# Optimization experiments

Hardware: AMD Instinct MI355X
Metric: run time of the kernel (lower is better)

## Reference

```python
import jax, jax.numpy as jnp
import numpy as np

N, NFEAT, NHID, NCLASS, NHEADS = 3072, 128, 64, 64, 8
ALPHA = 0.2  # LeakyReLU negative slope
NEG = -9e15  # masking value from pyGAT


def gat_layer(h, mask, W, a):
    # h: [N, Fin]; mask: [N, N] bool; W: [H, Fin, Fout]; a: [H, 2*Fout]
    fout = W.shape[-1]
    Wh = jnp.einsum('ni,hio->hno', h, W)            # [H, N, Fout]
    e_src = jnp.einsum('hno,ho->hn', Wh, a[:, :fout])
    e_dst = jnp.einsum('hno,ho->hn', Wh, a[:, fout:])
    e = jax.nn.leaky_relu(e_src[:, :, None] + e_dst[:, None, :], ALPHA)  # [H,N,N]
    e = jnp.where(mask[None], e, NEG)
    att = jax.nn.softmax(e, axis=-1)                 # dropout is identity in eval
    out = jnp.einsum('hnm,hmo->hno', att, Wh)        # [H, N, Fout]
    out = jax.nn.elu(out)                            # concat=True -> elu
    # concat heads along feature dim: [N, H*Fout]
    return out.transpose(1, 0, 2).reshape(h.shape[0], -1)


def setup_inputs() -> dict:
    key = jax.random.key(0)
    ks = jax.random.split(key, 10)
    x = jax.random.normal(ks[0], (N, NFEAT), dtype=jnp.float32)
    adj = (jax.random.uniform(ks[1], (N, N)) < 0.01).astype(jnp.float32)
    adj = jnp.maximum(adj, jnp.eye(N, dtype=jnp.float32))
    hid = NHID * NHEADS
    dims = [(NFEAT, NHID), (hid, NHID), (hid, NHID), (hid, NCLASS)]
    params = {}
    for i, (fin, fout) in enumerate(dims):
        kw, ka = jax.random.split(ks[2 + i])
        params[f'W{i+1}'] = jax.random.normal(kw, (NHEADS, fin, fout), dtype=jnp.float32) * (1.0 / np.sqrt(fin))
        params[f'a{i+1}'] = jax.random.normal(ka, (NHEADS, 2 * fout), dtype=jnp.float32) * 0.1
    return {'x': x, 'adj': adj, **params}


def reference(x, adj, W1, a1, W2, a2, W3, a3, W4, a4):
    mask = adj > 0
    h = gat_layer(x, mask, W1, a1)
    h = gat_layer(h, mask, W2, a2)
    h = gat_layer(h, mask, W3, a3)
    h = gat_layer(h, mask, W4, a4)
    return h  # [N, NHEADS*NCLASS]
```

## Files before the change

kernel.cpp:

```cpp
#include <hip/hip_runtime.h>
#include <math.h>

#define NN 3072
#define NH 8
#define FO 64
#define FCAT 512
#define MAXDEG 128
#define ALPHA 0.2f

typedef __attribute__((ext_vector_type(8))) short bf16x8;
typedef __attribute__((ext_vector_type(4))) float f32x4;

static __device__ __forceinline__ unsigned short f2bf(float v) {
    union { float f; unsigned u; } x; x.f = v;
    unsigned r = x.u + 0x7fffu + ((x.u >> 16) & 1u);
    return (unsigned short)(r >> 16);
}
static __device__ __forceinline__ float bf2f(unsigned short b) {
    union { unsigned u; float f; } x; x.u = ((unsigned)b) << 16;
    return x.f;
}

__global__ __launch_bounds__(256) void prelude_k(const float* __restrict__ x,
                                                 const float* __restrict__ adj,
                                                 const float* __restrict__ W1,
                                                 const float* __restrict__ W2,
                                                 const float* __restrict__ W3,
                                                 const float* __restrict__ W4,
                                                 unsigned short* __restrict__ Ah,
                                                 unsigned short* __restrict__ Al,
                                                 unsigned short* __restrict__ Wth,
                                                 unsigned short* __restrict__ Wtl,
                                                 int* __restrict__ deg,
                                                 int* __restrict__ nbr) {
    __shared__ float t[64][65];
    const int b = blockIdx.x, tid = threadIdx.x;

    if (b < 256) {
        int base = b * 1536 + tid;
        #pragma unroll
        for (int i = 0; i < 6; ++i) {
            int idx = base + i * 256;
            float v = x[idx];
            unsigned short hb = f2bf(v);
            Ah[idx] = hb;
            Al[idx] = f2bf(v - bf2f(hb));
        }
        if (b < 208) {
            const float* W; int K; int local; size_t obase;
            if (b < 16)       { W = W1; K = 128; local = b;       obase = 0; }
            else if (b < 80)  { W = W2; K = 512; local = b - 16;  obase = 65536; }
            else if (b < 144) { W = W3; K = 512; local = b - 80;  obase = 327680; }
            else              { W = W4; K = 512; local = b - 144; obase = 589824; }
            int nkt = K >> 6;
            int h = local / nkt, kt = local - h * nkt;
            int k0 = kt * 64;
            for (int idx = tid; idx < 4096; idx += 256) {
                int r = idx >> 6, c = idx & 63;
                t[r][c] = W[(size_t)h * K * FO + (size_t)(k0 + r) * FO + c];
            }
            __syncthreads();
            for (int idx = tid; idx < 4096; idx += 256) {
                int o = idx >> 6, kk = idx & 63;
                float v = t[kk][o];
                unsigned short hb = f2bf(v);
                size_t dst = obase + (size_t)(h * FO + o) * K + k0 + kk;
                Wth[dst] = hb;
                Wtl[dst] = f2bf(v - bf2f(hb));
            }
        }
    } else {
        int row = (b - 256) * 4 + (tid >> 6);
        int lane = tid & 63;
        const float* arow = adj + (size_t)row * NN;
        int count = 0;
        for (int base = 0; base < NN; base += 64) {
            float v = arow[base + lane];
            unsigned long long m = __ballot(v > 0.0f);
            if (v > 0.0f) {
                int pos = count + __popcll(m & ((1ull << lane) - 1ull));
                if (pos < MAXDEG) nbr[(size_t)row * MAXDEG + pos] = base + lane;
            }
            count += __popcll(m);
        }
        if (lane == 0) deg[row] = count < MAXDEG ? count : MAXDEG;
    }
}

__global__ __launch_bounds__(256, 3) void gemm_ee_k(const unsigned short* __restrict__ Ah,
                                                    const unsigned short* __restrict__ Al,
                                                    const unsigned short* __restrict__ Bh,
                                                    const unsigned short* __restrict__ Bl,
                                                    const float* __restrict__ a,
                                                    float* __restrict__ C,
                                                    float* __restrict__ esrc,
                                                    float* __restrict__ edst, int K) {
    __shared__ __align__(16) unsigned char smem[30720];
    typedef float CsT[68];
    unsigned short* As_ = (unsigned short*)smem;
    unsigned short* Bs_ = (unsigned short*)(smem + 10240);
    CsT* Cs = reinterpret_cast<CsT*>(smem);

    const int tid = threadIdx.x;
    const int h = blockIdx.x;
    const int r0 = blockIdx.y * 32;
    const int lane = tid & 63;
    const int wid = tid >> 6;
    const int wr = wid >> 1, wc = wid & 1;
    const int lr = lane & 15, lg = lane >> 4;

    const unsigned short* Bhh = Bh + (size_t)h * FO * K;
    const unsigned short* Bll = Bl + (size_t)h * FO * K;

    const int row0 = tid >> 3, cq0 = tid & 7;
    const int off0 = row0 * 80 + ((cq0 ^ (row0 & 7)) * 8);
    const size_t gA0 = (size_t)(r0 + row0) * K + cq0 * 8;
    const size_t gB0 = (size_t)row0 * K + cq0 * 8;
    const size_t gB1 = gB0 + (size_t)32 * K;

    bf16x8 rah, ral, rb0h, rb0l, rb1h, rb1l;

    auto loadg = [&](int k0) {
        rah = *(const bf16x8*)(Ah + gA0 + k0);
        ral = *(const bf16x8*)(Al + gA0 + k0);
        rb0h = *(const bf16x8*)(Bhh + gB0 + k0);
        rb0l = *(const bf16x8*)(Bll + gB0 + k0);
        rb1h = *(const bf16x8*)(Bhh + gB1 + k0);
        rb1l = *(const bf16x8*)(Bll + gB1 + k0);
    };
    auto store_lds = [&]() {
        *(bf16x8*)&As_[off0] = rah;
        *(bf16x8*)&As_[2560 + off0] = ral;
        *(bf16x8*)&Bs_[off0] = rb0h;
        *(bf16x8*)&Bs_[5120 + off0] = rb0l;
        *(bf16x8*)&Bs_[off0 + 2560] = rb1h;
        *(bf16x8*)&Bs_[5120 + off0 + 2560] = rb1l;
    };

    f32x4 acc[2];
    acc[0] = (f32x4){0.f, 0.f, 0.f, 0.f};
    acc[1] = (f32x4){0.f, 0.f, 0.f, 0.f};

    auto mfma_phase = [&]() {
        #pragma unroll
        for (int ks = 0; ks < 2; ++ks) {
            int cq = ks * 4 + lg;
            int arow = wr * 16 + lr;
            int offa = arow * 80 + ((cq ^ (arow & 7)) * 8);
            bf16x8 ah = *(const bf16x8*)&As_[offa];
            bf16x8 al = *(const bf16x8*)&As_[2560 + offa];
            bf16x8 bh[2], bl[2];
            #pragma unroll
            for (int j = 0; j < 2; ++j) {
                int col = wc * 32 + j * 16 + lr;
                int offb = col * 80 + ((cq ^ (col & 7)) * 8);
                bh[j] = *(const bf16x8*)&Bs_[offb];
                bl[j] = *(const bf16x8*)&Bs_[5120 + offb];
            }
            #pragma unroll
            for (int j = 0; j < 2; ++j) {
                acc[j] = __builtin_amdgcn_mfma_f32_16x16x32_bf16(ah, bh[j], acc[j], 0, 0, 0);
                acc[j] = __builtin_amdgcn_mfma_f32_16x16x32_bf16(ah, bl[j], acc[j], 0, 0, 0);
                acc[j] = __builtin_amdgcn_mfma_f32_16x16x32_bf16(al, bh[j], acc[j], 0, 0, 0);
            }
        }
    };

    loadg(0);
    store_lds();
    __syncthreads();
    for (int k0 = 64; k0 < K; k0 += 64) {
        loadg(k0);
        mfma_phase();
        __syncthreads();
        store_lds();
        __syncthreads();
    }
    mfma_phase();
    __syncthreads();

    #pragma unroll
    for (int j = 0; j < 2; ++j)
        #pragma unroll
        for (int r = 0; r < 4; ++r)
            Cs[wr * 16 + lg * 4 + r][wc * 32 + j * 16 + lr] = acc[j][r];
    __syncthreads();

    #pragma unroll
    for (int it = 0; it < 2; ++it) {
        int idx = tid + it * 256;
        int r = idx >> 4, c4 = idx & 15;
        *(float4*)&C[(size_t)(r0 + r) * FCAT + h * FO + c4 * 4] = *(float4*)&Cs[r][c4 * 4];
    }

    {
        int r = tid >> 3, sub = tid & 7;
        const float* av = a + h * 2 * FO;
        float s = 0.0f, dd = 0.0f;
        #pragma unroll
        for (int k = 0; k < 8; ++k) {
            float v = Cs[r][sub * 8 + k];
            s = fmaf(v, av[sub * 8 + k], s);
            dd = fmaf(v, av[FO + sub * 8 + k], dd);
        }
        s += __shfl_xor(s, 1); s += __shfl_xor(s, 2); s += __shfl_xor(s, 4);
        dd += __shfl_xor(dd, 1); dd += __shfl_xor(dd, 2); dd += __shfl_xor(dd, 4);
        if (sub == 0) {
            esrc[h * NN + r0 + r] = s;
            edst[h * NN + r0 + r] = dd;
        }
    }
}

__global__ __launch_bounds__(256) void attn_agg_k(const float* __restrict__ Wh,
                                                  const float* __restrict__ esrc,
                                                  const float* __restrict__ edst,
                                                  const int* __restrict__ deg,
                                                  const int* __restrict__ nbr,
                                                  float* __restrict__ outp,
                                                  unsigned short* __restrict__ oh,
                                                  unsigned short* __restrict__ ol,
                                                  int write_f32) {
    __shared__ float pbuf[4][MAXDEG];
    __shared__ int jbuf[4][MAXDEG];
    const int ws = threadIdx.x >> 6;
    const int lane = threadIdx.x & 63;
    const int h = blockIdx.x / (NN / 4);
    const int n = (blockIdx.x % (NN / 4)) * 4 + ws;
    const int d = deg[n];
    const int dpad = (d + 7) & ~7;
    const int* nb = nbr + (size_t)n * MAXDEG;
    const float es = esrc[h * NN + n];
    const float* ed = edst + h * NN;

    float lsum = 0.0f;
    for (int t = lane; t < dpad; t += 64) {
        int j = 0;
        float pv = 0.0f;
        if (t < d) {
            j = nb[t];
            float e = es + ed[j];
            e = (e > 0.0f) ? e : ALPHA * e;
            pv = __expf(e);
        }
        jbuf[ws][t] = j;
        pbuf[ws][t] = pv;
        lsum += pv;
    }
    #pragma unroll
    for (int off = 32; off; off >>= 1) lsum += __shfl_xor(lsum, off);

    const float* whb = Wh + h * FO + lane;
    float a0 = 0.f, a1 = 0.f, a2 = 0.f, a3 = 0.f;
    float a4 = 0.f, a5 = 0.f, a6 = 0.f, a7 = 0.f;
    for (int t = 0; t < dpad; t += 8) {
        a0 = fmaf(pbuf[ws][t + 0], whb[(size_t)jbuf[ws][t + 0] * FCAT], a0);
        a1 = fmaf(pbuf[ws][t + 1], whb[(size_t)jbuf[ws][t + 1] * FCAT], a1);
        a2 = fmaf(pbuf[ws][t + 2], whb[(size_t)jbuf[ws][t + 2] * FCAT], a2);
        a3 = fmaf(pbuf[ws][t + 3], whb[(size_t)jbuf[ws][t + 3] * FCAT], a3);
        a4 = fmaf(pbuf[ws][t + 4], whb[(size_t)jbuf[ws][t + 4] * FCAT], a4);
        a5 = fmaf(pbuf[ws][t + 5], whb[(size_t)jbuf[ws][t + 5] * FCAT], a5);
        a6 = fmaf(pbuf[ws][t + 6], whb[(size_t)jbuf[ws][t + 6] * FCAT], a6);
        a7 = fmaf(pbuf[ws][t + 7], whb[(size_t)jbuf[ws][t + 7] * FCAT], a7);
    }
    float acc = ((a0 + a1) + (a2 + a3)) + ((a4 + a5) + (a6 + a7));
    acc /= lsum;
    float r = (acc > 0.0f) ? acc : (__expf(acc) - 1.0f);
    size_t idx = (size_t)n * FCAT + h * FO + lane;
    if (write_f32) {
        outp[idx] = r;
    } else {
        unsigned short hb = f2bf(r);
        oh[idx] = hb;
        ol[idx] = f2bf(r - bf2f(hb));
    }
}

extern "C" void kernel_launch(void* const* d_in, const int* in_sizes, int n_in,
                              void* d_out, int out_size, void* d_ws, size_t ws_size,
                              hipStream_t stream) {
    const float* x   = (const float*)d_in[0];
    const float* adj = (const float*)d_in[1];
    const float* ap[4] = {(const float*)d_in[3], (const float*)d_in[5],
                          (const float*)d_in[7], (const float*)d_in[9]};
    float* out = (float*)d_out;

    char* p = (char*)d_ws;
    int* deg = (int*)p;              p += (size_t)NN * sizeof(int);
    int* nbr = (int*)p;              p += (size_t)NN * MAXDEG * sizeof(int);
    unsigned short* Ah = (unsigned short*)p; p += (size_t)NN * FCAT * 2;
    unsigned short* Al = (unsigned short*)p; p += (size_t)NN * FCAT * 2;
    float* WhF = (float*)p;          p += (size_t)NN * FCAT * sizeof(float);
    unsigned short* Wth = (unsigned short*)p; p += (size_t)851968 * 2;
    unsigned short* Wtl = (unsigned short*)p; p += (size_t)851968 * 2;
    float* esrc = (float*)p;         p += (size_t)NN * NH * sizeof(float);
    float* edst = (float*)p;         p += (size_t)NN * NH * sizeof(float);

    prelude_k<<<1024, 256, 0, stream>>>(x, adj,
                                        (const float*)d_in[2], (const float*)d_in[4],
                                        (const float*)d_in[6], (const float*)d_in[8],
                                        Ah, Al, Wth, Wtl, deg, nbr);

    const size_t woff[4] = {0, 65536, 327680, 589824};
    int K = 128;
    for (int L = 0; L < 4; ++L) {
        dim3 g(NH, NN / 32);
        gemm_ee_k<<<g, 256, 0, stream>>>(Ah, Al, Wth + woff[L], Wtl + woff[L],
                                         ap[L], WhF, esrc, edst, K);
        attn_agg_k<<<NH * (NN / 4), 256, 0, stream>>>(WhF, esrc, edst, deg, nbr,
                                                      out, Ah, Al, L == 3 ? 1 : 0);
        K = FCAT;
    }
}
```

Baseline: 135.1 us.

## Process all heads per wave in attention aggregation with interleaved edge scores

Restructures the attention-aggregation kernel so each wavefront handles one node across all 8 heads, with each lane owning 8 contiguous output columns. Neighbor indices are loaded once per node instead of once per head, and each gathered neighbor row is read with float4 loads covering the full 512-wide concat row. Edge scores are stored node-major and interleaved (src and dst per head) so a neighbor's scores sit in one 64-byte span. This cuts redundant neighbor-list reads and makes the gather loads wider. In exchange it launches 8x fewer blocks and uses more registers and shared memory per wave.

```diff
diff --git a/kernel.cpp b/kernel.cpp
--- a/kernel.cpp
+++ b/kernel.cpp
@@ -93,8 +93,7 @@
                                                     const unsigned short* __restrict__ Bl,
                                                     const float* __restrict__ a,
                                                     float* __restrict__ C,
-                                                    float* __restrict__ esrc,
-                                                    float* __restrict__ edst, int K) {
+                                                    float* __restrict__ ee, int K) {
     __shared__ __align__(16) unsigned char smem[30720];
     typedef float CsT[68];
     unsigned short* As_ = (unsigned short*)smem;
@@ -206,73 +205,112 @@
         s += __shfl_xor(s, 1); s += __shfl_xor(s, 2); s += __shfl_xor(s, 4);
         dd += __shfl_xor(dd, 1); dd += __shfl_xor(dd, 2); dd += __shfl_xor(dd, 4);
         if (sub == 0) {
-            esrc[h * NN + r0 + r] = s;
-            edst[h * NN + r0 + r] = dd;
+            ee[(size_t)(r0 + r) * 16 + h] = s;
+            ee[(size_t)(r0 + r) * 16 + 8 + h] = dd;
         }
     }
 }
 
 __global__ __launch_bounds__(256) void attn_agg_k(const float* __restrict__ Wh,
-                                                  const float* __restrict__ esrc,
-                                                  const float* __restrict__ edst,
+                                                  const float* __restrict__ ee,
                                                   const int* __restrict__ deg,
                                                   const int* __restrict__ nbr,
                                                   float* __restrict__ outp,
                                                   unsigned short* __restrict__ oh,
                                                   unsigned short* __restrict__ ol,
                                                   int write_f32) {
-    __shared__ float pbuf[4][MAXDEG];
     __shared__ int jbuf[4][MAXDEG];
+    __shared__ float pbuf[4][NH][MAXDEG + 4];
     const int ws = threadIdx.x >> 6;
     const int lane = threadIdx.x & 63;
-    const int h = blockIdx.x / (NN / 4);
-    const int n = (blockIdx.x % (NN / 4)) * 4 + ws;
+    const int n = blockIdx.x * 4 + ws;
+    const int head = lane >> 3;
+    const int tt = lane & 7;
     const int d = deg[n];
     const int dpad = (d + 7) & ~7;
     const int* nb = nbr + (size_t)n * MAXDEG;
-    const float es = esrc[h * NN + n];
-    const float* ed = edst + h * NN;
-
+
+    for (int t = lane; t < dpad; t += 64) jbuf[ws][t] = (t < d) ? nb[t] : 0;
+
+    const float es_h = ee[(size_t)n * 16 + head];
     float lsum = 0.0f;
-    for (int t = lane; t < dpad; t += 64) {
-        int j = 0;
+    for (int base = 0; base < dpad; base += 8) {
+        int t = base + tt;
+        int j = jbuf[ws][t];
         float pv = 0.0f;
         if (t < d) {
-            j = nb[t];
-            float e = es + ed[j];
+            float e = es_h + ee[(size_t)j * 16 + 8 + head];
             e = (e > 0.0f) ? e : ALPHA * e;
             pv = __expf(e);
         }
-        jbuf[ws][t] = j;
-        pbuf[ws][t] = pv;
+        pbuf[ws][head][t] = pv;
         lsum += pv;
     }
-    #pragma unroll
-    for (int off = 32; off; off >>= 1) lsum += __shfl_xor(lsum, off);
-
-    const float* whb = Wh + h * FO + lane;
+    lsum += __shfl_xor(lsum, 1);
+    lsum += __shfl_xor(lsum, 2);
+    lsum += __shfl_xor(lsum, 4);
+
+    const int coff = lane * 8;
     float a0 = 0.f, a1 = 0.f, a2 = 0.f, a3 = 0.f;
     float a4 = 0.f, a5 = 0.f, a6 = 0.f, a7 = 0.f;
-    for (int t = 0; t < dpad; t += 8) {
-        a0 = fmaf(pbuf[ws][t + 0], whb[(size_t)jbuf[ws][t + 0] * FCAT], a0);
-        a1 = fmaf(pbuf[ws][t + 1], whb[(size_t)jbuf[ws][t + 1] * FCAT], a1);
-        a2 = fmaf(pbuf[ws][t + 2], whb[(size_t)jbuf[ws][t + 2] * FCAT], a2);
-        a3 = fmaf(pbuf[ws][t + 3], whb[(size_t)jbuf[ws][t + 3] * FCAT], a3);
-        a4 = fmaf(pbuf[ws][t + 4], whb[(size_t)jbuf[ws][t + 4] * FCAT], a4);
-        a5 = fmaf(pbuf[ws][t + 5], whb[(size_t)jbuf[ws][t + 5] * FCAT], a5);
-        a6 = fmaf(pbuf[ws][t + 6], whb[(size_t)jbuf[ws][t + 6] * FCAT], a6);
-        a7 = fmaf(pbuf[ws][t + 7], whb[(size_t)jbuf[ws][t + 7] * FCAT], a7);
-    }
-    float acc = ((a0 + a1) + (a2 + a3)) + ((a4 + a5) + (a6 + a7));
-    acc /= lsum;
-    float r = (acc > 0.0f) ? acc : (__expf(acc) - 1.0f);
-    size_t idx = (size_t)n * FCAT + h * FO + lane;
+    for (int t = 0; t < dpad; t += 4) {
+        int4 jv = *(const int4*)&jbuf[ws][t];
+        float4 pv = *(const float4*)&pbuf[ws][head][t];
+        const float* r0 = Wh + (size_t)jv.x * FCAT + coff;
+        const float* r1 = Wh + (size_t)jv.y * FCAT + coff;
+        const float* r2 = Wh + (size_t)jv.z * FCAT + coff;
+        const float* r3 = Wh + (size_t)jv.w * FCAT + coff;
+        float4 v00 = *(const float4*)r0, v01 = *(const float4*)(r0 + 4);
+        float4 v10 = *(const float4*)r1, v11 = *(const float4*)(r1 + 4);
+        float4 v20 = *(const float4*)r2, v21 = *(const float4*)(r2 + 4);
+        float4 v30 = *(const float4*)r3, v31 = *(const float4*)(r3 + 4);
+        a0 = fmaf(pv.x, v00.x, a0); a1 = fmaf(pv.x, v00.y, a1);
+        a2 = fmaf(pv.x, v00.z, a2); a3 = fmaf(pv.x, v00.w, a3);
+        a4 = fmaf(pv.x, v01.x, a4); a5 = fmaf(pv.x, v01.y, a5);
+        a6 = fmaf(pv.x, v01.z, a6); a7 = fmaf(pv.x, v01.w, a7);
+        a0 = fmaf(pv.y, v10.x, a0); a1 = fmaf(pv.y, v10.y, a1);
+        a2 = fmaf(pv.y, v10.z, a2); a3 = fmaf(pv.y, v10.w, a3);
+        a4 = fmaf(pv.y, v11.x, a4); a5 = fmaf(pv.y, v11.y, a5);
+        a6 = fmaf(pv.y, v11.z, a6); a7 = fmaf(pv.y, v11.w, a7);
+        a0 = fmaf(pv.z, v20.x, a0); a1 = fmaf(pv.z, v20.y, a1);
+        a2 = fmaf(pv.z, v20.z, a2); a3 = fmaf(pv.z, v20.w, a3);
+        a4 = fmaf(pv.z, v21.x, a4); a5 = fmaf(pv.z, v21.y, a5);
+        a6 = fmaf(pv.z, v21.z, a6); a7 = fmaf(pv.z, v21.w, a7);
+        a0 = fmaf(pv.w, v30.x, a0); a1 = fmaf(pv.w, v30.y, a1);
+        a2 = fmaf(pv.w, v30.z, a2); a3 = fmaf(pv.w, v30.w, a3);
+        a4 = fmaf(pv.w, v31.x, a4); a5 = fmaf(pv.w, v31.y, a5);
+        a6 = fmaf(pv.w, v31.z, a6); a7 = fmaf(pv.w, v31.w, a7);
+    }
+
+    float inv = 1.0f / lsum;
+    float o0 = a0 * inv, o1 = a1 * inv, o2 = a2 * inv, o3 = a3 * inv;
+    float o4 = a4 * inv, o5 = a5 * inv, o6 = a6 * inv, o7 = a7 * inv;
+    o0 = (o0 > 0.f) ? o0 : (__expf(o0) - 1.f);
+    o1 = (o1 > 0.f) ? o1 : (__expf(o1) - 1.f);
+    o2 = (o2 > 0.f) ? o2 : (__expf(o2) - 1.f);
+    o3 = (o3 > 0.f) ? o3 : (__expf(o3) - 1.f);
+    o4 = (o4 > 0.f) ? o4 : (__expf(o4) - 1.f);
+    o5 = (o5 > 0.f) ? o5 : (__expf(o5) - 1.f);
+    o6 = (o6 > 0.f) ? o6 : (__expf(o6) - 1.f);
+    o7 = (o7 > 0.f) ? o7 : (__expf(o7) - 1.f);
+
+    size_t idx = (size_t)n * FCAT + coff;
     if (write_f32) {
-        outp[idx] = r;
+        float4 w0 = {o0, o1, o2, o3}, w1 = {o4, o5, o6, o7};
+        *(float4*)&outp[idx] = w0;
+        *(float4*)&outp[idx + 4] = w1;
     } else {
-        unsigned short hb = f2bf(r);
-        oh[idx] = hb;
-        ol[idx] = f2bf(r - bf2f(hb));
+        unsigned short h0 = f2bf(o0), h1 = f2bf(o1), h2 = f2bf(o2), h3 = f2bf(o3);
+        unsigned short h4 = f2bf(o4), h5 = f2bf(o5), h6 = f2bf(o6), h7 = f2bf(o7);
+        ushort4 hv0 = {h0, h1, h2, h3}, hv1 = {h4, h5, h6, h7};
+        ushort4 lv0 = {f2bf(o0 - bf2f(h0)), f2bf(o1 - bf2f(h1)),
+                       f2bf(o2 - bf2f(h2)), f2bf(o3 - bf2f(h3))};
+        ushort4 lv1 = {f2bf(o4 - bf2f(h4)), f2bf(o5 - bf2f(h5)),
+                       f2bf(o6 - bf2f(h6)), f2bf(o7 - bf2f(h7))};
+        *(ushort4*)&oh[idx] = hv0;
+        *(ushort4*)&oh[idx + 4] = hv1;
+        *(ushort4*)&ol[idx] = lv0;
+        *(ushort4*)&ol[idx + 4] = lv1;
     }
 }
 
@@ -293,8 +331,7 @@
     float* WhF = (float*)p;          p += (size_t)NN * FCAT * sizeof(float);
     unsigned short* Wth = (unsigned short*)p; p += (size_t)851968 * 2;
     unsigned short* Wtl = (unsigned short*)p; p += (size_t)851968 * 2;
-    float* esrc = (float*)p;         p += (size_t)NN * NH * sizeof(float);
-    float* edst = (float*)p;         p += (size_t)NN * NH * sizeof(float);
+    float* ee = (float*)p;           p += (size_t)NN * 16 * sizeof(float);
 
     prelude_k<<<1024, 256, 0, stream>>>(x, adj,
                                         (const float*)d_in[2], (const float*)d_in[4],
@@ -306,9 +343,9 @@
     for (int L = 0; L < 4; ++L) {
         dim3 g(NH, NN / 32);
         gemm_ee_k<<<g, 256, 0, stream>>>(Ah, Al, Wth + woff[L], Wtl + woff[L],
-                                         ap[L], WhF, esrc, edst, K);
-        attn_agg_k<<<NH * (NN / 4), 256, 0, stream>>>(WhF, esrc, edst, deg, nbr,
-                                                      out, Ah, Al, L == 3 ? 1 : 0);
+                                         ap[L], WhF, ee, K);
+        attn_agg_k<<<NN / 4, 256, 0, stream>>>(WhF, ee, deg, nbr,
+                                               out, Ah, Al, L == 3 ? 1 : 0);
         K = FCAT;
     }
 }
```

New measurement: 131.8 us, median of 2. 2.5% less time.
